# Kernel optimization log

Hardware: AMD Instinct MI355X
Metric: run time of the kernel (lower is better)

## Reference

```python
import jax, jax.numpy as jnp
import numpy as np

B, S, HIDDEN = 1, 2048, 2048
HEADS, HEAD_DIM = 32, 128
EPS = 1e-5
THETA = 10000.0


def setup_inputs() -> dict:
    key = jax.random.key(0)
    k0, k1, k2 = jax.random.split(key, 3)
    hidden_states = jax.random.normal(k0, (B, S, HIDDEN), jnp.float32)
    positions = jnp.broadcast_to(jnp.arange(S, dtype=jnp.int32)[None, :], (B, S))
    qkv_w = jax.random.normal(k1, (3 * HEADS * HEAD_DIM, HIDDEN), jnp.float32) * 0.02
    q_norm_w = jnp.ones((HEAD_DIM,), jnp.float32)
    k_norm_w = jnp.ones((HEAD_DIM,), jnp.float32)
    o_proj_w = jax.random.normal(k2, (HIDDEN, HEADS * HEAD_DIM), jnp.float32) * 0.02
    return {"hidden_states": hidden_states, "positions": positions, "qkv_w": qkv_w,
            "q_norm_w": q_norm_w, "k_norm_w": k_norm_w, "o_proj_w": o_proj_w}


def _rmsnorm(x, w):
    # RMSNorm over last (head_dim) axis
    var = jnp.mean(x * x, axis=-1, keepdims=True)
    return x * jax.lax.rsqrt(var + EPS) * w


def _rope(x, positions):
    # NeoX-style (non-interleaved) rotary over full head_dim
    d2 = HEAD_DIM // 2
    inv_freq = 1.0 / (THETA ** (jnp.arange(0, HEAD_DIM, 2, dtype=jnp.float32) / HEAD_DIM))
    freqs = positions.astype(jnp.float32)[..., None] * inv_freq  # [B,S,d2]
    cos = jnp.cos(freqs)[:, :, None, :]  # [B,S,1,d2]
    sin = jnp.sin(freqs)[:, :, None, :]
    x1, x2 = x[..., :d2], x[..., d2:]
    return jnp.concatenate([x1 * cos - x2 * sin, x2 * cos + x1 * sin], axis=-1)


def reference(hidden_states, positions, qkv_w, q_norm_w, k_norm_w, o_proj_w):
    b, s, _ = hidden_states.shape
    qkv = jnp.einsum('bsh,oh->bso', hidden_states, qkv_w)  # [B,S,3*H*D]
    q, k, v = jnp.split(qkv, 3, axis=-1)
    q = q.reshape(b, s, HEADS, HEAD_DIM)
    k = k.reshape(b, s, HEADS, HEAD_DIM)
    v = v.reshape(b, s, HEADS, HEAD_DIM)
    # qk_norm (per-head RMSNorm)
    q = _rmsnorm(q, q_norm_w)
    k = _rmsnorm(k, k_norm_w)
    # rotary embedding
    q = _rope(q, positions)
    k = _rope(k, positions)
    # causal attention, scale = head_dim**-0.5 (flash_attn default)
    scale = HEAD_DIM ** -0.5
    scores = jnp.einsum('bqhd,bkhd->bhqk', q, k) * scale  # [B,H,S,S]
    causal = jnp.tril(jnp.ones((s, s), dtype=bool))
    scores = jnp.where(causal[None, None], scores, jnp.float32(-1e30))
    probs = jax.nn.softmax(scores, axis=-1)
    o = jnp.einsum('bhqk,bkhd->bqhd', probs, v).reshape(b, s, HEADS * HEAD_DIM)
    return jnp.einsum('bso,ho->bsh', o, o_proj_w)
```

## Files before the change

kernel.cpp:

```cpp
#include <hip/hip_runtime.h>
#include <cstdint>
#include <cstddef>

static constexpr int S_LEN = 2048;
static constexpr int HID   = 2048;
static constexpr int NH    = 32;
static constexpr int HD    = 128;
static constexpr int OD    = 4096;
static constexpr int QKV_O = 12288;

#define AS1 __attribute__((address_space(1)))
#define AS3 __attribute__((address_space(3)))

typedef __attribute__((ext_vector_type(8))) short bf16x8;
typedef __attribute__((ext_vector_type(4))) float f32x4;
typedef __attribute__((ext_vector_type(4))) short s16x4;

template <int V> struct IC { static constexpr int v = V; };

__device__ __forceinline__ short f2bf(float f) {
  unsigned u = __float_as_uint(f);
  unsigned r = (u + 0x7fffu + ((u >> 16) & 1u)) >> 16;
  return (short)r;
}
__device__ __forceinline__ float bf2f(short s) {
  return __uint_as_float(((unsigned)(unsigned short)s) << 16);
}
__device__ __forceinline__ unsigned pk2bf(float a, float b) {
  return __builtin_amdgcn_perm(__float_as_uint(b), __float_as_uint(a), 0x07060302u);
}

__global__ void convert2_kernel(const float* __restrict__ in1, short* __restrict__ out1, int n1_4,
                                const float* __restrict__ in2, short* __restrict__ out2, int n2_4) {
  int i = blockIdx.x * blockDim.x + threadIdx.x;
  const float* in; short* out; int j;
  if (i < n1_4) { in = in1; out = out1; j = i; }
  else { j = i - n1_4; if (j >= n2_4) return; in = in2; out = out2; }
  float4 f = ((const float4*)in)[j];
  s16x4 s;
  s.x = f2bf(f.x); s.y = f2bf(f.y); s.z = f2bf(f.z); s.w = f2bf(f.w);
  ((s16x4*)out)[j] = s;
}

template <int BNT, int CMODE>
__global__ __launch_bounds__(512, 2) void gemm8p(
    const short* __restrict__ A, const short* __restrict__ Bw, void* __restrict__ Cp,
    int K, int N, int ldc) {
  constexpr int BH  = BNT / 128;
  constexpr int NJ  = BNT / 64;
  constexpr int NJH = NJ / 2;
  __shared__ short Al[2][128 * 64];
  __shared__ short Bl[2][BH][128 * 64];
  const int tid  = threadIdx.x;
  const int lane = tid & 63;
  const int quad = lane >> 4;
  const int col  = lane & 15;
  const int wave = tid >> 6;
  const int wm   = wave >> 2;
  const int wn   = wave & 3;

  const int nbn = N / BNT;
  const int nbm = gridDim.x / nbn;
  const int xcd = blockIdx.x & 7;
  const int u   = blockIdx.x >> 3;
  const int m0  = (u % nbm) * 128;
  const int n0  = (xcd * (nbn >> 3) + u / nbm) * BNT;

  const int NT = K >> 6;

  f32x4 acc[4][NJ] = {};
  bf16x8 a[4][2], b0[NJH][2], b1[NJH][2];

  auto stA = [&](int t, int buf) {
#pragma unroll
    for (int r = 0; r < 2; ++r) {
      int idx = r * 512 + tid;
      int row = idx >> 3;
      int g   = idx & 7;
      int gs  = g ^ ((row >> 1) & 7);
      const short* ga = A + (size_t)(m0 + row) * K + t * 64 + gs * 8;
      __builtin_amdgcn_global_load_lds((const AS1 unsigned*)ga,
                                       (AS3 unsigned*)&Al[buf][idx * 8], 16, 0, 0);
    }
  };
  auto stB = [&](int t, int buf, int h) {
#pragma unroll
    for (int r = 0; r < 2; ++r) {
      int idx = r * 512 + tid;
      int row = idx >> 3;
      int g   = idx & 7;
      int gs  = g ^ ((row >> 1) & 7);
      const short* gb = Bw + (size_t)(n0 + h * 128 + row) * K + t * 64 + gs * 8;
      __builtin_amdgcn_global_load_lds((const AS1 unsigned*)gb,
                                       (AS3 unsigned*)&Bl[buf][h][idx * 8], 16, 0, 0);
    }
  };
  auto rdA = [&](int buf, int mh) {
#pragma unroll
    for (int i = 0; i < 2; ++i) {
      int rh = wm * 64 + (mh * 2 + i) * 16 + col;
#pragma unroll
      for (int kf = 0; kf < 2; ++kf)
        a[mh * 2 + i][kf] =
            *(const bf16x8*)&Al[buf][rh * 64 + (((kf * 4 + quad) ^ ((rh >> 1) & 7)) * 8)];
    }
  };
  auto rdB = [&](int buf, int nh, bf16x8 (&bb)[NJH][2]) {
#pragma unroll
    for (int j = 0; j < NJH; ++j) {
      int br = wn * (BNT / 4) + nh * (BNT / 8) + j * 16 + col;
      int bh = br >> 7, rh = br & 127;
#pragma unroll
      for (int kf = 0; kf < 2; ++kf)
        bb[j][kf] =
            *(const bf16x8*)&Bl[buf][bh][rh * 64 + (((kf * 4 + quad) ^ ((rh >> 1) & 7)) * 8)];
    }
  };
  auto mm = [&](auto MH, auto NHc, bf16x8 (&bb)[NJH][2]) {
    constexpr int mh = MH.v, nh = NHc.v;
    __builtin_amdgcn_s_setprio(1);
#pragma unroll
    for (int i = 0; i < 2; ++i)
#pragma unroll
      for (int j = 0; j < NJH; ++j)
#pragma unroll
        for (int kf = 0; kf < 2; ++kf)
          acc[mh * 2 + i][nh * NJH + j] = __builtin_amdgcn_mfma_f32_16x16x32_bf16(
              a[mh * 2 + i][kf], bb[j][kf], acc[mh * 2 + i][nh * NJH + j], 0, 0, 0);
    __builtin_amdgcn_s_setprio(0);
  };
#define LGK() do { asm volatile("s_waitcnt lgkmcnt(0)"); __builtin_amdgcn_sched_barrier(0); } while (0)
#define BAR() __builtin_amdgcn_s_barrier()
  auto vmc_mid = [] {
    if constexpr (BH == 1) asm volatile("s_waitcnt vmcnt(4)" ::: "memory");
    else                   asm volatile("s_waitcnt vmcnt(6)" ::: "memory");
  };
  auto vmc_end = [] {
    if constexpr (BH == 1)      asm volatile("s_waitcnt vmcnt(4)" ::: "memory");
    else if constexpr (BH == 2) asm volatile("s_waitcnt vmcnt(6)" ::: "memory");
    else                        asm volatile("s_waitcnt vmcnt(8)" ::: "memory");
  };

#pragma unroll
  for (int h = 0; h < BH; ++h) stB(0, 0, h);
  stA(0, 0);
#pragma unroll
  for (int h = 0; h < BH; ++h) stB(1, 1, h);
  stA(1, 1);
  if constexpr (BH == 1)      asm volatile("s_waitcnt vmcnt(4)" ::: "memory");
  else if constexpr (BH == 2) asm volatile("s_waitcnt vmcnt(6)" ::: "memory");
  else                        asm volatile("s_waitcnt vmcnt(8)" ::: "memory");
  BAR();

  for (int i = 0; i < (NT >> 1); ++i) {
    const int t  = 2 * i;
    const int tA = (t + 2 < NT) ? t + 2 : NT - 2;
    const int tB = (t + 3 < NT) ? t + 3 : NT - 1;
    rdA(0, 0); rdB(0, 0, b0);
    BAR(); LGK();
    mm(IC<0>{}, IC<0>{}, b0);
    BAR();
    rdB(0, 1, b1);
    BAR(); LGK();
    mm(IC<0>{}, IC<1>{}, b1);
    BAR();
    rdA(0, 1);
    stB(tA, 0, 0);
    BAR(); LGK();
    mm(IC<1>{}, IC<1>{}, b1);
    BAR();
    if constexpr (BH >= 2) stB(tA, 0, 1);
    stA(tA, 0);
    BAR();
    mm(IC<1>{}, IC<0>{}, b0);
    vmc_mid();
    BAR();
    rdA(1, 0); rdB(1, 0, b0);
    if constexpr (BH == 3) stB(tA, 0, 2);
    BAR(); LGK();
    mm(IC<0>{}, IC<0>{}, b0);
    BAR();
    rdB(1, 1, b1);
    BAR(); LGK();
    mm(IC<0>{}, IC<1>{}, b1);
    BAR();
    rdA(1, 1);
    stB(tB, 1, 0);
    if constexpr (BH >= 2) stB(tB, 1, 1);
    BAR(); LGK();
    mm(IC<1>{}, IC<1>{}, b1);
    BAR();
    if constexpr (BH == 3) stB(tB, 1, 2);
    stA(tB, 1);
    BAR();
    mm(IC<1>{}, IC<0>{}, b0);
    vmc_end();
    BAR();
  }
#undef LGK
#undef BAR

#pragma unroll
  for (int mi = 0; mi < 4; ++mi)
#pragma unroll
    for (int nj = 0; nj < NJ; ++nj)
#pragma unroll
      for (int r = 0; r < 4; ++r) {
        int rr = m0 + wm * 64 + mi * 16 + quad * 4 + r;
        int cc = n0 + wn * (BNT / 4) + nj * 16 + col;
        if (CMODE == 1)
          ((float*)Cp)[(size_t)rr * ldc + cc] = acc[mi][nj][r];
        else
          ((short*)Cp)[(size_t)rr * ldc + cc] = f2bf(acc[mi][nj][r]);
      }
}

#define BM 128
#define BK 32

template <int BNT, int CMODE>
__global__ __launch_bounds__(256, 2) void gemm_nt_f32w(
    const short* __restrict__ A, const float* __restrict__ B, void* __restrict__ Cp,
    int K, int ldc) {
  __shared__ short Alds[2][BM * BK];
  __shared__ short Blds[2][BNT * BK];
  constexpr int WN  = BNT / 2;
  constexpr int NJ  = WN / 16;
  constexpr int BCH = (BNT * 4) / 256;
  const int tid  = threadIdx.x;
  const int lane = tid & 63;
  const int quad = lane >> 4;
  const int col  = lane & 15;
  const int wave = tid >> 6;
  const int m0 = blockIdx.y * BM;
  const int n0 = blockIdx.x * BNT;
  const int wm = (wave & 1) * 64;
  const int wn = (wave >> 1) * WN;

  f32x4 acc[4][NJ] = {};
  float4 breg[BCH][2];

  const int nk = K / BK;

  auto b_issue = [&](int k0) {
#pragma unroll
    for (int it = 0; it < BCH; ++it) {
      int idx = it * 256 + tid;
      int row = idx >> 2;
      int c   = idx & 3;
      const float* gb = B + (size_t)(n0 + row) * K + k0 + c * 8;
      breg[it][0] = *(const float4*)gb;
      breg[it][1] = *(const float4*)(gb + 4);
    }
  };
  auto a_issue = [&](int k0, int buf) {
#pragma unroll
    for (int it = 0; it < 2; ++it) {
      int idx = it * 256 + tid;
      int row = idx >> 2;
      int c   = idx & 3;
      int cs  = c ^ ((row >> 1) & 3);
      const short* ga = A + (size_t)(m0 + row) * K + k0 + cs * 8;
      __builtin_amdgcn_global_load_lds((const AS1 unsigned*)ga,
                                       (AS3 unsigned*)&Alds[buf][idx * 8], 16, 0, 0);
    }
  };
  auto b_write = [&](int buf) {
#pragma unroll
    for (int it = 0; it < BCH; ++it) {
      int idx = it * 256 + tid;
      int row = idx >> 2;
      int c   = idx & 3;
      int cw  = c ^ ((row >> 1) & 3);
      union { unsigned u[4]; bf16x8 v; } pk;
      pk.u[0] = pk2bf(breg[it][0].x, breg[it][0].y);
      pk.u[1] = pk2bf(breg[it][0].z, breg[it][0].w);
      pk.u[2] = pk2bf(breg[it][1].x, breg[it][1].y);
      pk.u[3] = pk2bf(breg[it][1].z, breg[it][1].w);
      *(bf16x8*)&Blds[buf][(row * 4 + cw) * 8] = pk.v;
    }
  };
  auto compute = [&](int buf) {
    bf16x8 a[4], b[NJ];
#pragma unroll
    for (int i = 0; i < 4; ++i) {
      int row = wm + i * 16 + col;
      a[i] = *(const bf16x8*)&Alds[buf][(row * 4 + (quad ^ ((row >> 1) & 3))) * 8];
    }
#pragma unroll
    for (int j = 0; j < NJ; ++j) {
      int row = wn + j * 16 + col;
      b[j] = *(const bf16x8*)&Blds[buf][(row * 4 + (quad ^ ((row >> 1) & 3))) * 8];
    }
#pragma unroll
    for (int i = 0; i < 4; ++i)
#pragma unroll
      for (int j = 0; j < NJ; ++j)
        acc[i][j] = __builtin_amdgcn_mfma_f32_16x16x32_bf16(a[i], b[j], acc[i][j], 0, 0, 0);
  };

  b_issue(0);
  a_issue(0, 0);
  b_write(0);
  __syncthreads();

  for (int t = 0; t < nk - 1; ++t) {
    const int cur = t & 1;
    b_issue((t + 1) * BK);
    a_issue((t + 1) * BK, cur ^ 1);
    compute(cur);
    b_write(cur ^ 1);
    __syncthreads();
  }
  compute((nk - 1) & 1);

#pragma unroll
  for (int i = 0; i < 4; ++i)
#pragma unroll
    for (int j = 0; j < NJ; ++j)
#pragma unroll
      for (int r = 0; r < 4; ++r) {
        int rr = m0 + wm + i * 16 + quad * 4 + r;
        int cc = n0 + wn + j * 16 + col;
        if (CMODE == 1)
          ((float*)Cp)[(size_t)rr * ldc + cc] = acc[i][j][r];
        else
          ((short*)Cp)[(size_t)rr * ldc + cc] = f2bf(acc[i][j][r]);
      }
}

__global__ void normrope_packv_kernel(short* __restrict__ qkv,
                                      const int* __restrict__ positions,
                                      const float* __restrict__ qw,
                                      const float* __restrict__ kw,
                                      short* __restrict__ vtp) {
  __shared__ short T[64][136];
  if (blockIdx.x < 32768) {
    int item = blockIdx.x * 4 + (threadIdx.x >> 6);
    int lane = threadIdx.x & 63;
    int head  = item & 31;
    int which = (item >> 5) & 1;
    int s     = item >> 6;
    const float* w = which ? kw : qw;
    short* base = qkv + (size_t)s * QKV_O + which * OD + head * HD;

    float x1 = bf2f(base[lane]);
    float x2 = bf2f(base[lane + 64]);
    float ss = x1 * x1 + x2 * x2;
#pragma unroll
    for (int d = 32; d; d >>= 1) ss += __shfl_xor(ss, d);
    float r = rsqrtf(ss * (1.0f / 128.0f) + 1e-5f);
    float xn1 = x1 * r * w[lane];
    float xn2 = x2 * r * w[lane + 64];

    float pos = (float)positions[s];
    float inv_freq = exp2f((float)lane * (-13.287712379549449f / 64.0f));
    float f = pos * inv_freq;
    float c = cosf(f), sn = sinf(f);
    float sc = which ? 1.0f : 0.12751863738f;
    base[lane]      = f2bf((xn1 * c - xn2 * sn) * sc);
    base[lane + 64] = f2bf((xn2 * c + xn1 * sn) * sc);
  } else {
    int bid2 = blockIdx.x - 32768;
    const int h  = bid2 & 31;
    const int kt = bid2 >> 5;
    const int tid = threadIdx.x;
    {
      int rr = tid >> 2;
      int db = (tid & 3) * 32;
      const short* src = qkv + (size_t)(kt * 64 + rr) * QKV_O + 2 * OD + h * HD + db;
#pragma unroll
      for (int i = 0; i < 4; ++i)
        *(bf16x8*)&T[rr][db + i * 8] = *(const bf16x8*)(src + i * 8);
    }
    __syncthreads();
    {
      int d  = tid >> 1;
      int k0 = (tid & 1) * 32;
      short* dst = vtp + (((size_t)h * 32 + kt) * 128 + d) * 64 + k0;
#pragma unroll
      for (int c = 0; c < 4; ++c) {
        bf16x8 v;
#pragma unroll
        for (int j = 0; j < 8; ++j) v[j] = T[k0 + c * 8 + j][d];
        *(bf16x8*)&dst[c * 8] = v;
      }
    }
  }
}

__global__ __launch_bounds__(256, 3) void attn_kernel(
    const short* __restrict__ qkv, const short* __restrict__ vtp, short* __restrict__ obuf) {
  __shared__ short Klds[64 * 128];
  __shared__ short Vt[128 * 64];
  __shared__ short Plds[4][16 * 64];

  const int tid  = threadIdx.x;
  const int lane = tid & 63;
  const int wave = tid >> 6;
  const int quad = lane >> 4;
  const int col  = lane & 15;
  const int h    = blockIdx.y;

  const int kr  = tid >> 2;
  const int kcb = (tid & 3) * 32;
  const int vd  = tid >> 1;
  const int vcb = (tid & 1) * 32;

  bf16x8 kreg[4], vreg[4];

  auto loadK = [&](int kt) {
    const short* kp = qkv + (size_t)(kt * 64 + kr) * QKV_O + OD + h * HD + kcb;
#pragma unroll
    for (int i = 0; i < 4; ++i) kreg[i] = *(const bf16x8*)(kp + i * 8);
  };
  auto loadV = [&](int kt) {
    const short* vp = vtp + (((size_t)h * 32 + kt) * 128 + vd) * 64 + vcb;
#pragma unroll
    for (int i = 0; i < 4; ++i) vreg[i] = *(const bf16x8*)(vp + i * 8);
  };
  auto writeKV = [&]() {
#pragma unroll
    for (int i = 0; i < 4; ++i) {
      int swz = ((tid & 3) * 4 + i) ^ (kr & 15);
      *(bf16x8*)&Klds[kr * 128 + swz * 8] = kreg[i];
    }
#pragma unroll
    for (int i = 0; i < 4; ++i) {
      int swz = ((tid & 1) * 4 + i) ^ (vd & 7);
      *(bf16x8*)&Vt[vd * 64 + swz * 8] = vreg[i];
    }
  };

#pragma unroll 1
  for (int half = 0; half < 2; ++half) {
    const int qt = half == 0 ? blockIdx.x : 31 - blockIdx.x;
    const int qbase = qt * 64 + wave * 16;

    bf16x8 qf[4];
#pragma unroll
    for (int kf = 0; kf < 4; ++kf)
      qf[kf] = *(const bf16x8*)(qkv + (size_t)(qbase + col) * QKV_O + h * HD + kf * 32 + quad * 8);

    f32x4 o[8] = {};
    float m_r[4], l_i[4];
#pragma unroll
    for (int r = 0; r < 4; ++r) { m_r[r] = -1e30f; l_i[r] = 0.f; }

    loadK(0); loadV(0);

#pragma unroll 1
    for (int kt = 0; kt <= qt; ++kt) {
      __syncthreads();
      writeKV();
      __syncthreads();
      if (kt < qt) { loadK(kt + 1); loadV(kt + 1); }

      f32x4 sfr[4];
      __builtin_amdgcn_s_setprio(1);
#pragma unroll
      for (int nf = 0; nf < 4; ++nf) {
        f32x4 acc = {};
#pragma unroll
        for (int kf = 0; kf < 4; ++kf) {
          bf16x8 b = *(const bf16x8*)&Klds[(nf * 16 + col) * 128 + ((kf * 4 + quad) ^ col) * 8];
          acc = __builtin_amdgcn_mfma_f32_16x16x32_bf16(qf[kf], b, acc, 0, 0, 0);
        }
        sfr[nf] = acc;
      }
      __builtin_amdgcn_s_setprio(0);

      if (kt == qt) {
#pragma unroll
        for (int nf = 0; nf < 4; ++nf)
#pragma unroll
          for (int r = 0; r < 4; ++r) {
            int key = kt * 64 + nf * 16 + col;
            int qg  = qbase + quad * 4 + r;
            if (key > qg) sfr[nf][r] = -1e30f;
          }
      }

#pragma unroll
      for (int r = 0; r < 4; ++r) {
        float mt = fmaxf(fmaxf(sfr[0][r], sfr[1][r]), fmaxf(sfr[2][r], sfr[3][r]));
#pragma unroll
        for (int d = 8; d; d >>= 1) mt = fmaxf(mt, __shfl_xor(mt, d));
        float mnew = fmaxf(m_r[r], mt);
        bool defer = __all(mnew - m_r[r] <= 8.0f);
        if (defer) mnew = m_r[r];
        float alpha = exp2f(m_r[r] - mnew);
        float ps = 0.f;
#pragma unroll
        for (int nf = 0; nf < 4; ++nf) {
          float p = exp2f(sfr[nf][r] - mnew);
          sfr[nf][r] = p;
          ps += p;
        }
        l_i[r] = l_i[r] * alpha + ps;
        if (!defer) {
#pragma unroll
          for (int nf = 0; nf < 8; ++nf) o[nf][r] *= alpha;
          m_r[r] = mnew;
        }
      }

#pragma unroll
      for (int nf = 0; nf < 4; ++nf)
#pragma unroll
        for (int r = 0; r < 4; ++r) {
          int row = quad * 4 + r;
          int key = nf * 16 + col;
          Plds[wave][row * 64 + ((key >> 3) ^ (row & 7)) * 8 + (key & 7)] = f2bf(sfr[nf][r]);
        }

      bf16x8 pa[2];
#pragma unroll
      for (int kf = 0; kf < 2; ++kf)
        pa[kf] = *(const bf16x8*)&Plds[wave][col * 64 + ((kf * 4 + quad) ^ (col & 7)) * 8];
      __builtin_amdgcn_s_setprio(1);
#pragma unroll
      for (int nf = 0; nf < 8; ++nf)
#pragma unroll
        for (int kf = 0; kf < 2; ++kf) {
          bf16x8 vb = *(const bf16x8*)&Vt[(nf * 16 + col) * 64 + ((kf * 4 + quad) ^ (col & 7)) * 8];
          o[nf] = __builtin_amdgcn_mfma_f32_16x16x32_bf16(pa[kf], vb, o[nf], 0, 0, 0);
        }
      __builtin_amdgcn_s_setprio(0);
    }

#pragma unroll
    for (int r = 0; r < 4; ++r) {
      float lt = l_i[r];
#pragma unroll
      for (int d = 8; d; d >>= 1) lt += __shfl_xor(lt, d);
      float inv = 1.0f / lt;
      int sg = qbase + quad * 4 + r;
#pragma unroll
      for (int nf = 0; nf < 8; ++nf)
        obuf[(size_t)sg * OD + h * HD + nf * 16 + col] = f2bf(o[nf][r] * inv);
    }
  }
}

extern "C" void kernel_launch(void* const* d_in, const int* in_sizes, int n_in,
                              void* d_out, int out_size, void* d_ws, size_t ws_size,
                              hipStream_t stream) {
  (void)in_sizes; (void)n_in; (void)out_size;
  const float* hs   = (const float*)d_in[0];
  const int*   pos  = (const int*)d_in[1];
  const float* qkvw = (const float*)d_in[2];
  const float* qw   = (const float*)d_in[3];
  const float* kw   = (const float*)d_in[4];
  const float* ow   = (const float*)d_in[5];
  float* out = (float*)d_out;

  char* ws = (char*)d_ws;
  short* qkvb    = (short*)(ws);
  short* obuf    = (short*)(ws + 50331648);
  short* qkvw_bf = (short*)(ws + 67108864);
  short* ow_bf   = (short*)(ws + 67108864);
  short* hsb  = (short*)d_out;
  short* vtp  = (short*)d_out;

  const bool fast = ws_size >= (size_t)117440512;

  if (fast) {
    int n1 = (S_LEN * HID) / 4, n2 = (QKV_O * HID) / 4;
    convert2_kernel<<<(n1 + n2 + 255) / 256, 256, 0, stream>>>(hs, hsb, n1, qkvw, qkvw_bf, n2);
    gemm8p<256, 0><<<(S_LEN / 128) * (QKV_O / 256), 512, 0, stream>>>(
        hsb, qkvw_bf, qkvb, HID, QKV_O, QKV_O);
    int n3 = (HID * OD) / 4;
    convert2_kernel<<<(n3 + 255) / 256, 256, 0, stream>>>(ow, ow_bf, n3, ow, ow_bf, 0);
  } else {
    int n1 = (S_LEN * HID) / 4;
    convert2_kernel<<<(n1 + 255) / 256, 256, 0, stream>>>(hs, hsb, n1, hs, hsb, 0);
    gemm_nt_f32w<128, 0><<<dim3(QKV_O / 128, S_LEN / BM), 256, 0, stream>>>(
        hsb, qkvw, qkvb, HID, QKV_O);
  }

  normrope_packv_kernel<<<(S_LEN * 2 * NH) / 4 + NH * (S_LEN / 64), 256, 0, stream>>>(
      qkvb, pos, qw, kw, vtp);

  attn_kernel<<<dim3(16, NH), 256, 0, stream>>>(qkvb, vtp, obuf);

  if (fast) {
    gemm8p<128, 1><<<(S_LEN / 128) * (HID / 128), 512, 0, stream>>>(
        obuf, ow_bf, out, OD, HID, HID);
  } else {
    gemm_nt_f32w<64, 1><<<dim3(HID / 64, S_LEN / BM), 256, 0, stream>>>(
        obuf, ow, out, OD, HID);
  }
}
```

Baseline: 490.7 us.

## Use 256x256 QKV GEMM tiles, fuse o_proj conversion, double-buffer attention KV

Makes the GEMM M-tile a template parameter and launches the QKV projection with 256x256 tiles, giving more reuse per loaded tile at the cost of more accumulator registers and LDS. The o_proj weight fp32-to-bf16 conversion moves into extra blocks of the norm/rope kernel, which removes one launch. The attention kernel double-buffers K/V in LDS so the next tile's global loads overlap compute, with one fewer barrier per iteration. Occupancy is lowered to 2 because of the doubled LDS.

```diff
diff --git a/kernel.cpp b/kernel.cpp
--- a/kernel.cpp
+++ b/kernel.cpp
@@ -42,14 +42,17 @@
   ((s16x4*)out)[j] = s;
 }
 
-template <int BNT, int CMODE>
+template <int BMt, int BNT, int CMODE>
 __global__ __launch_bounds__(512, 2) void gemm8p(
     const short* __restrict__ A, const short* __restrict__ Bw, void* __restrict__ Cp,
     int K, int N, int ldc) {
   constexpr int BH  = BNT / 128;
   constexpr int NJ  = BNT / 64;
   constexpr int NJH = NJ / 2;
-  __shared__ short Al[2][128 * 64];
+  constexpr int MF  = BMt / 64;
+  constexpr int AST = BMt / 64;
+  constexpr int LT  = 2 * (BMt / 128) + 2 * BH;
+  __shared__ short Al[2][BMt * 64];
   __shared__ short Bl[2][BH][128 * 64];
   const int tid  = threadIdx.x;
   const int lane = tid & 63;
@@ -63,17 +66,17 @@
   const int nbm = gridDim.x / nbn;
   const int xcd = blockIdx.x & 7;
   const int u   = blockIdx.x >> 3;
-  const int m0  = (u % nbm) * 128;
+  const int m0  = (u % nbm) * BMt;
   const int n0  = (xcd * (nbn >> 3) + u / nbm) * BNT;
 
   const int NT = K >> 6;
 
-  f32x4 acc[4][NJ] = {};
-  bf16x8 a[4][2], b0[NJH][2], b1[NJH][2];
+  f32x4 acc[2 * MF][NJ] = {};
+  bf16x8 a[MF][2], b0[NJH][2], b1[NJH][2];
 
   auto stA = [&](int t, int buf) {
 #pragma unroll
-    for (int r = 0; r < 2; ++r) {
+    for (int r = 0; r < AST; ++r) {
       int idx = r * 512 + tid;
       int row = idx >> 3;
       int g   = idx & 7;
@@ -97,11 +100,11 @@
   };
   auto rdA = [&](int buf, int mh) {
 #pragma unroll
-    for (int i = 0; i < 2; ++i) {
-      int rh = wm * 64 + (mh * 2 + i) * 16 + col;
+    for (int i = 0; i < MF; ++i) {
+      int rh = wm * (BMt / 2) + (mh * MF + i) * 16 + col;
 #pragma unroll
       for (int kf = 0; kf < 2; ++kf)
-        a[mh * 2 + i][kf] =
+        a[i][kf] =
             *(const bf16x8*)&Al[buf][rh * 64 + (((kf * 4 + quad) ^ ((rh >> 1) & 7)) * 8)];
     }
   };
@@ -120,25 +123,21 @@
     constexpr int mh = MH.v, nh = NHc.v;
     __builtin_amdgcn_s_setprio(1);
 #pragma unroll
-    for (int i = 0; i < 2; ++i)
+    for (int i = 0; i < MF; ++i)
 #pragma unroll
       for (int j = 0; j < NJH; ++j)
 #pragma unroll
         for (int kf = 0; kf < 2; ++kf)
-          acc[mh * 2 + i][nh * NJH + j] = __builtin_amdgcn_mfma_f32_16x16x32_bf16(
-              a[mh * 2 + i][kf], bb[j][kf], acc[mh * 2 + i][nh * NJH + j], 0, 0, 0);
+          acc[mh * MF + i][nh * NJH + j] = __builtin_amdgcn_mfma_f32_16x16x32_bf16(
+              a[i][kf], bb[j][kf], acc[mh * MF + i][nh * NJH + j], 0, 0, 0);
     __builtin_amdgcn_s_setprio(0);
   };
 #define LGK() do { asm volatile("s_waitcnt lgkmcnt(0)"); __builtin_amdgcn_sched_barrier(0); } while (0)
 #define BAR() __builtin_amdgcn_s_barrier()
-  auto vmc_mid = [] {
-    if constexpr (BH == 1) asm volatile("s_waitcnt vmcnt(4)" ::: "memory");
-    else                   asm volatile("s_waitcnt vmcnt(6)" ::: "memory");
-  };
-  auto vmc_end = [] {
-    if constexpr (BH == 1)      asm volatile("s_waitcnt vmcnt(4)" ::: "memory");
-    else if constexpr (BH == 2) asm volatile("s_waitcnt vmcnt(6)" ::: "memory");
-    else                        asm volatile("s_waitcnt vmcnt(8)" ::: "memory");
+  auto vmc = [] {
+    if constexpr (LT == 8)      asm volatile("s_waitcnt vmcnt(8)" ::: "memory");
+    else if constexpr (LT == 6) asm volatile("s_waitcnt vmcnt(6)" ::: "memory");
+    else                        asm volatile("s_waitcnt vmcnt(4)" ::: "memory");
   };
 
 #pragma unroll
@@ -147,9 +146,7 @@
 #pragma unroll
   for (int h = 0; h < BH; ++h) stB(1, 1, h);
   stA(1, 1);
-  if constexpr (BH == 1)      asm volatile("s_waitcnt vmcnt(4)" ::: "memory");
-  else if constexpr (BH == 2) asm volatile("s_waitcnt vmcnt(6)" ::: "memory");
-  else                        asm volatile("s_waitcnt vmcnt(8)" ::: "memory");
+  vmc();
   BAR();
 
   for (int i = 0; i < (NT >> 1); ++i) {
@@ -173,10 +170,9 @@
     stA(tA, 0);
     BAR();
     mm(IC<1>{}, IC<0>{}, b0);
-    vmc_mid();
+    vmc();
     BAR();
     rdA(1, 0); rdB(1, 0, b0);
-    if constexpr (BH == 3) stB(tA, 0, 2);
     BAR(); LGK();
     mm(IC<0>{}, IC<0>{}, b0);
     BAR();
@@ -190,23 +186,22 @@
     BAR(); LGK();
     mm(IC<1>{}, IC<1>{}, b1);
     BAR();
-    if constexpr (BH == 3) stB(tB, 1, 2);
     stA(tB, 1);
     BAR();
     mm(IC<1>{}, IC<0>{}, b0);
-    vmc_end();
+    vmc();
     BAR();
   }
 #undef LGK
 #undef BAR
 
 #pragma unroll
-  for (int mi = 0; mi < 4; ++mi)
+  for (int mi = 0; mi < 2 * MF; ++mi)
 #pragma unroll
     for (int nj = 0; nj < NJ; ++nj)
 #pragma unroll
       for (int r = 0; r < 4; ++r) {
-        int rr = m0 + wm * 64 + mi * 16 + quad * 4 + r;
+        int rr = m0 + wm * (BMt / 2) + mi * 16 + quad * 4 + r;
         int cc = n0 + wn * (BNT / 4) + nj * 16 + col;
         if (CMODE == 1)
           ((float*)Cp)[(size_t)rr * ldc + cc] = acc[mi][nj][r];
@@ -333,7 +328,10 @@
                                       const int* __restrict__ positions,
                                       const float* __restrict__ qw,
                                       const float* __restrict__ kw,
-                                      short* __restrict__ vtp) {
+                                      short* __restrict__ vtp,
+                                      const float* __restrict__ ow,
+                                      short* __restrict__ ow_bf,
+                                      int n3_4) {
   __shared__ short T[64][136];
   if (blockIdx.x < 32768) {
     int item = blockIdx.x * 4 + (threadIdx.x >> 6);
@@ -360,7 +358,7 @@
     float sc = which ? 1.0f : 0.12751863738f;
     base[lane]      = f2bf((xn1 * c - xn2 * sn) * sc);
     base[lane + 64] = f2bf((xn2 * c + xn1 * sn) * sc);
-  } else {
+  } else if (blockIdx.x < 33792) {
     int bid2 = blockIdx.x - 32768;
     const int h  = bid2 & 31;
     const int kt = bid2 >> 5;
@@ -386,13 +384,20 @@
         *(bf16x8*)&dst[c * 8] = v;
       }
     }
+  } else {
+    int i = (blockIdx.x - 33792) * 256 + threadIdx.x;
+    if (i >= n3_4) return;
+    float4 f = ((const float4*)ow)[i];
+    s16x4 s;
+    s.x = f2bf(f.x); s.y = f2bf(f.y); s.z = f2bf(f.z); s.w = f2bf(f.w);
+    ((s16x4*)ow_bf)[i] = s;
   }
 }
 
-__global__ __launch_bounds__(256, 3) void attn_kernel(
+__global__ __launch_bounds__(256, 2) void attn_kernel(
     const short* __restrict__ qkv, const short* __restrict__ vtp, short* __restrict__ obuf) {
-  __shared__ short Klds[64 * 128];
-  __shared__ short Vt[128 * 64];
+  __shared__ short Klds[2][64 * 128];
+  __shared__ short Vt[2][128 * 64];
   __shared__ short Plds[4][16 * 64];
 
   const int tid  = threadIdx.x;
@@ -419,16 +424,16 @@
 #pragma unroll
     for (int i = 0; i < 4; ++i) vreg[i] = *(const bf16x8*)(vp + i * 8);
   };
-  auto writeKV = [&]() {
+  auto writeKV = [&](int buf) {
 #pragma unroll
     for (int i = 0; i < 4; ++i) {
       int swz = ((tid & 3) * 4 + i) ^ (kr & 15);
-      *(bf16x8*)&Klds[kr * 128 + swz * 8] = kreg[i];
+      *(bf16x8*)&Klds[buf][kr * 128 + swz * 8] = kreg[i];
     }
 #pragma unroll
     for (int i = 0; i < 4; ++i) {
       int swz = ((tid & 1) * 4 + i) ^ (vd & 7);
-      *(bf16x8*)&Vt[vd * 64 + swz * 8] = vreg[i];
+      *(bf16x8*)&Vt[buf][vd * 64 + swz * 8] = vreg[i];
     }
   };
 
@@ -448,13 +453,14 @@
     for (int r = 0; r < 4; ++r) { m_r[r] = -1e30f; l_i[r] = 0.f; }
 
     loadK(0); loadV(0);
+    __syncthreads();
+    writeKV(0);
 
 #pragma unroll 1
     for (int kt = 0; kt <= qt; ++kt) {
+      const int cur = kt & 1;
+      if (kt < qt) { loadK(kt + 1); loadV(kt + 1); }
       __syncthreads();
-      writeKV();
-      __syncthreads();
-      if (kt < qt) { loadK(kt + 1); loadV(kt + 1); }
 
       f32x4 sfr[4];
       __builtin_amdgcn_s_setprio(1);
@@ -463,7 +469,7 @@
         f32x4 acc = {};
 #pragma unroll
         for (int kf = 0; kf < 4; ++kf) {
-          bf16x8 b = *(const bf16x8*)&Klds[(nf * 16 + col) * 128 + ((kf * 4 + quad) ^ col) * 8];
+          bf16x8 b = *(const bf16x8*)&Klds[cur][(nf * 16 + col) * 128 + ((kf * 4 + quad) ^ col) * 8];
           acc = __builtin_amdgcn_mfma_f32_16x16x32_bf16(qf[kf], b, acc, 0, 0, 0);
         }
         sfr[nf] = acc;
@@ -523,10 +529,12 @@
       for (int nf = 0; nf < 8; ++nf)
 #pragma unroll
         for (int kf = 0; kf < 2; ++kf) {
-          bf16x8 vb = *(const bf16x8*)&Vt[(nf * 16 + col) * 64 + ((kf * 4 + quad) ^ (col & 7)) * 8];
+          bf16x8 vb = *(const bf16x8*)&Vt[cur][(nf * 16 + col) * 64 + ((kf * 4 + quad) ^ (col & 7)) * 8];
           o[nf] = __builtin_amdgcn_mfma_f32_16x16x32_bf16(pa[kf], vb, o[nf], 0, 0, 0);
         }
       __builtin_amdgcn_s_setprio(0);
+
+      if (kt < qt) writeKV(cur ^ 1);
     }
 
 #pragma unroll
@@ -568,24 +576,24 @@
   if (fast) {
     int n1 = (S_LEN * HID) / 4, n2 = (QKV_O * HID) / 4;
     convert2_kernel<<<(n1 + n2 + 255) / 256, 256, 0, stream>>>(hs, hsb, n1, qkvw, qkvw_bf, n2);
-    gemm8p<256, 0><<<(S_LEN / 128) * (QKV_O / 256), 512, 0, stream>>>(
+    gemm8p<256, 256, 0><<<(S_LEN / 256) * (QKV_O / 256), 512, 0, stream>>>(
         hsb, qkvw_bf, qkvb, HID, QKV_O, QKV_O);
     int n3 = (HID * OD) / 4;
-    convert2_kernel<<<(n3 + 255) / 256, 256, 0, stream>>>(ow, ow_bf, n3, ow, ow_bf, 0);
+    normrope_packv_kernel<<<(S_LEN * 2 * NH) / 4 + NH * (S_LEN / 64) + n3 / 256,
+                            256, 0, stream>>>(qkvb, pos, qw, kw, vtp, ow, ow_bf, n3);
   } else {
     int n1 = (S_LEN * HID) / 4;
     convert2_kernel<<<(n1 + 255) / 256, 256, 0, stream>>>(hs, hsb, n1, hs, hsb, 0);
     gemm_nt_f32w<128, 0><<<dim3(QKV_O / 128, S_LEN / BM), 256, 0, stream>>>(
         hsb, qkvw, qkvb, HID, QKV_O);
+    normrope_packv_kernel<<<(S_LEN * 2 * NH) / 4 + NH * (S_LEN / 64),
+                            256, 0, stream>>>(qkvb, pos, qw, kw, vtp, hs, (short*)d_ws, 0);
   }
 
-  normrope_packv_kernel<<<(S_LEN * 2 * NH) / 4 + NH * (S_LEN / 64), 256, 0, stream>>>(
-      qkvb, pos, qw, kw, vtp);
-
   attn_kernel<<<dim3(16, NH), 256, 0, stream>>>(qkvb, vtp, obuf);
 
   if (fast) {
-    gemm8p<128, 1><<<(S_LEN / 128) * (HID / 128), 512, 0, stream>>>(
+    gemm8p<128, 128, 1><<<(S_LEN / 128) * (HID / 128), 512, 0, stream>>>(
         obuf, ow_bf, out, OD, HID, HID);
   } else {
     gemm_nt_f32w<64, 1><<<dim3(HID / 64, S_LEN / BM), 256, 0, stream>>>(
```

Result: faster. 480.2 us (-2.1%).
